# Optimization experiments

Hardware: AMD Instinct MI355X
Metric: run time of the kernel (lower is better)

## Reference

```python
import jax, jax.numpy as jnp
import numpy as np

N_TOKENS = 4096
HIDDEN = 2048
INTER = 1024
N_EXPERTS = 8          # routed experts
ZERO_EXPERTS = 2       # Longcat zero-computation (identity) experts
TOP_K = 2
ROUTED_SCALING = 2.5


def setup_inputs() -> dict:
    key = jax.random.key(0)
    k1, k2, k3, k4 = jax.random.split(key, 4)
    hidden_states = jax.random.normal(k1, (N_TOKENS, HIDDEN), dtype=jnp.float32)
    router_w = jax.random.normal(k2, (N_EXPERTS + ZERO_EXPERTS, HIDDEN), dtype=jnp.float32) * 0.02
    correction_bias = jnp.zeros((N_EXPERTS + ZERO_EXPERTS,), dtype=jnp.float32)
    # torch Linear weight layout [out, in]: gate_up [E, 2I, H], down [E, H, I]
    w_gate_up = jax.random.normal(k3, (N_EXPERTS, 2 * INTER, HIDDEN), dtype=jnp.float32) * 0.02
    w_down = jax.random.normal(k4, (N_EXPERTS, HIDDEN, INTER), dtype=jnp.float32) * 0.02
    return {
        'hidden_states': hidden_states,
        'router_w': router_w,
        'correction_bias': correction_bias,
        'w_gate_up': w_gate_up,
        'w_down': w_down,
    }


def reference(hidden_states, router_w, correction_bias, w_gate_up, w_down):
    x = hidden_states  # [N, H]
    # ---- router gemm (fp32, like dsv3_router_gemm) ----
    logits = jnp.einsum('nh,eh->ne', x.astype(jnp.float32), router_w)  # [N, E+Z]
    scores = jax.nn.sigmoid(logits)
    # biased top-k selection (sglang biased topk, renormalize=False)
    _, topk_idx = jax.lax.top_k(scores + correction_bias[None, :], TOP_K)  # [N, K]
    topk_w = jnp.take_along_axis(scores, topk_idx, axis=1)  # raw sigmoid scores
    # ---- combine weights per expert ----
    onehot = jax.nn.one_hot(topk_idx, N_EXPERTS + ZERO_EXPERTS, dtype=topk_w.dtype)  # [N,K,E+Z]
    combine = jnp.einsum('nke,nk->ne', onehot, topk_w)  # [N, E+Z]
    combine_real = combine[:, :N_EXPERTS]               # [N, E]
    w_zero = combine[:, N_EXPERTS:].sum(axis=-1)        # [N] identity-expert weight
    # ---- expert FFN (silu(gate) * up -> down), dense over experts ----
    gu = jnp.einsum('nh,efh->enf', x, w_gate_up)        # [E, N, 2I]
    gate, up = gu[..., :INTER], gu[..., INTER:]
    h = jax.nn.silu(gate) * up                          # [E, N, I]
    y = jnp.einsum('eni,ehi->enh', h, w_down)           # [E, N, H]
    out = jnp.einsum('enh,ne->nh', y, combine_real.astype(y.dtype))
    out = out + w_zero[:, None].astype(out.dtype) * x   # zero experts = identity
    return out * ROUTED_SCALING
```

## Files before the change

### kernel.cpp

```cpp
#include <hip/hip_runtime.h>
#include <cstdint>
#include <cstddef>

#define N_TOKENS 4096
#define HIDDEN   2048
#define INTER    1024
#define NE       8
#define NE_TOT   10
#define SCALE    2.5f

typedef short v8s __attribute__((ext_vector_type(8)));
typedef float v4f __attribute__((ext_vector_type(4)));

static __device__ inline int imin(int a, int b) { return a < b ? a : b; }

__device__ inline unsigned short f2bf(float f) {
  unsigned int u = __float_as_uint(f);
  u += 0x7fffu + ((u >> 16) & 1u);
  return (unsigned short)(u >> 16);
}

__device__ inline void gld_lds16(const void* g, void* l) {
  __builtin_amdgcn_global_load_lds(
      (const __attribute__((address_space(1))) unsigned int*)g,
      (__attribute__((address_space(3))) unsigned int*)l, 16, 0, 0);
}

__global__ __launch_bounds__(256) void cvt_all_kernel(
    const float* __restrict__ wgu, const float* __restrict__ wd,
    unsigned short* __restrict__ wgu_b, unsigned short* __restrict__ wd_b,
    int* __restrict__ counts) {
  if (blockIdx.x == 0 && threadIdx.x < NE) counts[threadIdx.x] = 0;
  int i = blockIdx.x * 256 + threadIdx.x;
  const int n8_gu = NE * 2 * INTER * HIDDEN / 8;
  const int n8_d  = NE * HIDDEN * INTER / 8;
  const float* src;
  unsigned short* dst;
  size_t b;
  if (i < n8_gu)            { src = wgu; dst = wgu_b; b = (size_t)i * 8; }
  else if (i < n8_gu + n8_d){ src = wd;  dst = wd_b;  b = (size_t)(i - n8_gu) * 8; }
  else return;
  float4 a0 = *(const float4*)(src + b);
  float4 a1 = *(const float4*)(src + b + 4);
  union { unsigned short u[8]; uint4 v; } r;
  r.u[0] = f2bf(a0.x); r.u[1] = f2bf(a0.y); r.u[2] = f2bf(a0.z); r.u[3] = f2bf(a0.w);
  r.u[4] = f2bf(a1.x); r.u[5] = f2bf(a1.y); r.u[6] = f2bf(a1.z); r.u[7] = f2bf(a1.w);
  *(uint4*)(dst + b) = r.v;
}

__global__ __launch_bounds__(256, 4) void router_kernel(
    const float* __restrict__ x, const float* __restrict__ rw,
    const float* __restrict__ bias, unsigned short* __restrict__ xb,
    int* __restrict__ counts, int* __restrict__ tok_list,
    int* __restrict__ tkp, float* __restrict__ tkw, float* __restrict__ out) {
  int tid  = threadIdx.x;
  int lane = tid & 63;
  int wid  = tid >> 6;
  int n    = blockIdx.x * 4 + wid;

  const float* xr = x + (size_t)n * HIDDEN;
  float acc[NE_TOT];
#pragma unroll
  for (int e = 0; e < NE_TOT; e++) acc[e] = 0.f;

#pragma unroll 1
  for (int i = 0; i < 8; i++) {
    int k = (i * 64 + lane) * 4;
    float4 xv = *(const float4*)(xr + k);
#pragma unroll
    for (int e = 0; e < NE_TOT; e++) {
      float4 w = *(const float4*)(rw + (size_t)e * HIDDEN + k);
      acc[e] += xv.x * w.x + xv.y * w.y + xv.z * w.z + xv.w * w.w;
    }
  }
#pragma unroll
  for (int e = 0; e < NE_TOT; e++) {
    float v = acc[e];
#pragma unroll
    for (int off = 32; off > 0; off >>= 1) v += __shfl_xor(v, off, 64);
    acc[e] = v;
  }

  float sc[NE_TOT], sb[NE_TOT];
#pragma unroll
  for (int e = 0; e < NE_TOT; e++) {
    sc[e] = 1.f / (1.f + expf(-acc[e]));
    sb[e] = sc[e] + bias[e];
  }
  int i1 = 0;
  for (int e = 1; e < NE_TOT; e++) if (sb[e] > sb[i1]) i1 = e;
  int i2 = (i1 == 0) ? 1 : 0;
  for (int e = 0; e < NE_TOT; e++) if (e != i1 && sb[e] > sb[i2]) i2 = e;
  float wzero = 0.f;
  if (i1 >= NE) wzero += sc[i1];
  if (i2 >= NE) wzero += sc[i2];
  if (lane == 0) {
#pragma unroll
    for (int tt = 0; tt < 2; tt++) {
      int idx = tt == 0 ? i1 : i2;
      int packed = 0;
      float w = 0.f;
      if (idx < NE) {
        int slot = atomicAdd(&counts[idx], 1);
        tok_list[idx * N_TOKENS + slot] = n;
        packed = (idx << 16) | slot;
        w = SCALE * sc[idx];
      }
      tkp[tt * N_TOKENS + n] = packed;
      tkw[tt * N_TOKENS + n] = w;
    }
  }
  float wz = SCALE * wzero;

#pragma unroll
  for (int i = 0; i < 8; i++) {
    int k = (i * 64 + lane) * 4;
    float4 xv = *(const float4*)(xr + k);
    ushort4 ob;
    ob.x = f2bf(xv.x); ob.y = f2bf(xv.y);
    ob.z = f2bf(xv.z); ob.w = f2bf(xv.w);
    *(ushort4*)(xb + (size_t)n * HIDDEN + k) = ob;
    float4 o;
    o.x = wz * xv.x; o.y = wz * xv.y; o.z = wz * xv.z; o.w = wz * xv.w;
    *(float4*)(out + (size_t)n * HIDDEN + k) = o;
  }
}

__global__ void offsets_kernel(const int* __restrict__ counts, int* __restrict__ offsets) {
  if (threadIdx.x == 0) {
    int s = 0;
    for (int e = 0; e < NE; e++) { offsets[e] = s; s += counts[e]; }
  }
}


__global__ __launch_bounds__(256, 2) void gateup_kernel(
    const unsigned short* __restrict__ xb, const unsigned short* __restrict__ wgu,
    const int* __restrict__ counts, const int* __restrict__ offsets,
    const int* __restrict__ tok_list, unsigned short* __restrict__ h_buf) {
  int jt = blockIdx.x;
  int mt = blockIdx.y;
  int e  = blockIdx.z;
  int count = counts[e];
  if (mt * 128 >= count) return;

  __shared__ unsigned short As[2][128 * 32];
  __shared__ unsigned short Bs[2][128 * 32];

  int tid  = threadIdx.x;
  int lane = tid & 63;
  int wm = (tid >> 7) & 1;
  int wn = (tid >> 6) & 1;

  int row0 = tid >> 2, row1 = row0 + 64;
  int col8 = (((tid & 3) ^ ((tid >> 3) & 3)) * 8);

  const int* tl = tok_list + e * N_TOKENS;
  int t0 = tl[imin(mt * 128 + row0, count - 1)];
  int t1 = tl[imin(mt * 128 + row1, count - 1)];
  const unsigned short* ag0 = xb + (size_t)t0 * HIDDEN + col8;
  const unsigned short* ag1 = xb + (size_t)t1 * HIDDEN + col8;

  int wn0 = row0 >> 6, wi0 = row0 & 63;
  int wn1 = row1 >> 6, wi1 = row1 & 63;
  int br0 = (wi0 < 32) ? (jt * 64 + wn0 * 32 + wi0) : (1024 + jt * 64 + wn0 * 32 + (wi0 - 32));
  int br1 = (wi1 < 32) ? (jt * 64 + wn1 * 32 + wi1) : (1024 + jt * 64 + wn1 * 32 + (wi1 - 32));
  const unsigned short* bbase = wgu + (size_t)e * (2 * INTER) * HIDDEN;
  const unsigned short* bg0 = bbase + (size_t)br0 * HIDDEN + col8;
  const unsigned short* bg1 = bbase + (size_t)br1 * HIDDEN + col8;

  v4f acc[4][4];
#pragma unroll
  for (int i = 0; i < 4; i++)
#pragma unroll
    for (int j = 0; j < 4; j++) acc[i][j] = v4f{0.f, 0.f, 0.f, 0.f};

  int mrow = wm * 64 + (lane & 15);
  int nrow = wn * 64 + (lane & 15);
  int kcol = (((lane >> 4) ^ ((lane >> 1) & 3)) * 8);

  gld_lds16(ag0, &As[0][(size_t)tid * 8]);
  gld_lds16(ag1, &As[0][2048 + (size_t)tid * 8]);
  gld_lds16(bg0, &Bs[0][(size_t)tid * 8]);
  gld_lds16(bg1, &Bs[0][2048 + (size_t)tid * 8]);
  ag0 += 32; ag1 += 32; bg0 += 32; bg1 += 32;
  __syncthreads();

  const int NK = HIDDEN / 32;
  for (int kt = 0; kt < NK; kt++) {
    int cur = kt & 1;
    if (kt + 1 < NK) {
      int nxt = cur ^ 1;
      gld_lds16(ag0, &As[nxt][(size_t)tid * 8]);
      gld_lds16(ag1, &As[nxt][2048 + (size_t)tid * 8]);
      gld_lds16(bg0, &Bs[nxt][(size_t)tid * 8]);
      gld_lds16(bg1, &Bs[nxt][2048 + (size_t)tid * 8]);
      ag0 += 32; ag1 += 32; bg0 += 32; bg1 += 32;
    }
    v8s a[4], b[4];
#pragma unroll
    for (int i = 0; i < 4; i++) a[i] = *(const v8s*)&As[cur][(mrow + i * 16) * 32 + kcol];
#pragma unroll
    for (int j = 0; j < 4; j++) b[j] = *(const v8s*)&Bs[cur][(nrow + j * 16) * 32 + kcol];
#pragma unroll
    for (int i = 0; i < 4; i++)
#pragma unroll
      for (int j = 0; j < 4; j++)
        acc[i][j] = __builtin_amdgcn_mfma_f32_16x16x32_bf16(a[i], b[j], acc[i][j], 0, 0, 0);
    __syncthreads();
  }

  int ocol  = lane & 15;
  int orow4 = (lane >> 4) * 4;
  int hoff  = offsets[e];
#pragma unroll
  for (int i = 0; i < 4; i++) {
#pragma unroll
    for (int r = 0; r < 4; r++) {
      int m = mt * 128 + wm * 64 + i * 16 + orow4 + r;
      if (m < count) {
        unsigned short* hrow = h_buf + (size_t)(hoff + m) * INTER;
#pragma unroll
        for (int j = 0; j < 2; j++) {
          float g = acc[i][j][r];
          float u = acc[i][j + 2][r];
          float hv = (g / (1.f + expf(-g))) * u;
          hrow[jt * 64 + wn * 32 + j * 16 + ocol] = f2bf(hv);
        }
      }
    }
  }
}

__global__ __launch_bounds__(256, 2) void down_kernel(
    const unsigned short* __restrict__ h_buf, const unsigned short* __restrict__ wd,
    const int* __restrict__ counts, const int* __restrict__ offsets,
    float* __restrict__ y_buf) {
  int nt = blockIdx.x;
  int mt = blockIdx.y;
  int e  = blockIdx.z;
  int count = counts[e];
  if (mt * 128 >= count) return;

  __shared__ unsigned short As[2][128 * 32];
  __shared__ unsigned short Bs[2][128 * 32];

  int tid  = threadIdx.x;
  int lane = tid & 63;
  int wm = (tid >> 7) & 1;
  int wn = (tid >> 6) & 1;

  int row0 = tid >> 2, row1 = row0 + 64;
  int col8 = (((tid & 3) ^ ((tid >> 3) & 3)) * 8);
  int hoff = offsets[e];

  const unsigned short* ag0 =
      h_buf + (size_t)(hoff + imin(mt * 128 + row0, count - 1)) * INTER + col8;
  const unsigned short* ag1 =
      h_buf + (size_t)(hoff + imin(mt * 128 + row1, count - 1)) * INTER + col8;
  const unsigned short* bbase = wd + (size_t)e * HIDDEN * INTER;
  const unsigned short* bg0 = bbase + (size_t)(nt * 128 + row0) * INTER + col8;
  const unsigned short* bg1 = bbase + (size_t)(nt * 128 + row1) * INTER + col8;

  v4f acc[4][4];
#pragma unroll
  for (int i = 0; i < 4; i++)
#pragma unroll
    for (int j = 0; j < 4; j++) acc[i][j] = v4f{0.f, 0.f, 0.f, 0.f};

  int mrow = wm * 64 + (lane & 15);
  int nrow = wn * 64 + (lane & 15);
  int kcol = (((lane >> 4) ^ ((lane >> 1) & 3)) * 8);

  gld_lds16(ag0, &As[0][(size_t)tid * 8]);
  gld_lds16(ag1, &As[0][2048 + (size_t)tid * 8]);
  gld_lds16(bg0, &Bs[0][(size_t)tid * 8]);
  gld_lds16(bg1, &Bs[0][2048 + (size_t)tid * 8]);
  ag0 += 32; ag1 += 32; bg0 += 32; bg1 += 32;
  __syncthreads();

  const int NK = INTER / 32;
  for (int kt = 0; kt < NK; kt++) {
    int cur = kt & 1;
    if (kt + 1 < NK) {
      int nxt = cur ^ 1;
      gld_lds16(ag0, &As[nxt][(size_t)tid * 8]);
      gld_lds16(ag1, &As[nxt][2048 + (size_t)tid * 8]);
      gld_lds16(bg0, &Bs[nxt][(size_t)tid * 8]);
      gld_lds16(bg1, &Bs[nxt][2048 + (size_t)tid * 8]);
      ag0 += 32; ag1 += 32; bg0 += 32; bg1 += 32;
    }
    v8s a[4], b[4];
#pragma unroll
    for (int i = 0; i < 4; i++) a[i] = *(const v8s*)&As[cur][(mrow + i * 16) * 32 + kcol];
#pragma unroll
    for (int j = 0; j < 4; j++) b[j] = *(const v8s*)&Bs[cur][(nrow + j * 16) * 32 + kcol];
#pragma unroll
    for (int i = 0; i < 4; i++)
#pragma unroll
      for (int j = 0; j < 4; j++)
        acc[i][j] = __builtin_amdgcn_mfma_f32_16x16x32_bf16(a[i], b[j], acc[i][j], 0, 0, 0);
    __syncthreads();
  }

  int ocol  = lane & 15;
  int orow4 = (lane >> 4) * 4;
#pragma unroll
  for (int i = 0; i < 4; i++) {
#pragma unroll
    for (int r = 0; r < 4; r++) {
      int m = mt * 128 + wm * 64 + i * 16 + orow4 + r;
      if (m < count) {
        float* yrow = y_buf + (size_t)(hoff + m) * HIDDEN + nt * 128 + wn * 64 + ocol;
#pragma unroll
        for (int j = 0; j < 4; j++) yrow[j * 16] = acc[i][j][r];
      }
    }
  }
}

__global__ __launch_bounds__(256, 4) void gather_kernel(
    const float* __restrict__ y_buf, const int* __restrict__ tkp,
    const float* __restrict__ tkw, const int* __restrict__ offsets,
    float* __restrict__ out) {
  int tid  = threadIdx.x;
  int lane = tid & 63;
  int wid  = tid >> 6;
  int n    = blockIdx.x * 4 + wid;

  int p1 = tkp[n], p2 = tkp[N_TOKENS + n];
  float w1 = tkw[n], w2 = tkw[N_TOKENS + n];
  const float* y1 = y_buf + (size_t)(offsets[p1 >> 16] + (p1 & 0xffff)) * HIDDEN;
  const float* y2 = y_buf + (size_t)(offsets[p2 >> 16] + (p2 & 0xffff)) * HIDDEN;
  float* orow = out + (size_t)n * HIDDEN;

#pragma unroll
  for (int i = 0; i < 8; i++) {
    int k = (i * 64 + lane) * 4;
    float4 o = *(const float4*)(orow + k);
    float4 a = *(const float4*)(y1 + k);
    float4 b = *(const float4*)(y2 + k);
    o.x += w1 * a.x + w2 * b.x;
    o.y += w1 * a.y + w2 * b.y;
    o.z += w1 * a.z + w2 * b.z;
    o.w += w1 * a.w + w2 * b.w;
    *(float4*)(orow + k) = o;
  }
}

extern "C" void kernel_launch(void* const* d_in, const int* in_sizes, int n_in,
                              void* d_out, int out_size, void* d_ws, size_t ws_size,
                              hipStream_t stream) {
  const float* x   = (const float*)d_in[0];
  const float* rw  = (const float*)d_in[1];
  const float* cb  = (const float*)d_in[2];
  const float* wgu = (const float*)d_in[3];
  const float* wd  = (const float*)d_in[4];
  float* out = (float*)d_out;

  char* ws = (char*)d_ws;
  size_t off = 0;
  auto alloc = [&](size_t bytes) {
    void* p = ws + off;
    off += (bytes + 255) & ~(size_t)255;
    return p;
  };
  unsigned short* xb    = (unsigned short*)alloc((size_t)N_TOKENS * HIDDEN * 2);
  unsigned short* wgu_b = (unsigned short*)alloc((size_t)NE * 2 * INTER * HIDDEN * 2);
  unsigned short* wd_b  = (unsigned short*)alloc((size_t)NE * HIDDEN * INTER * 2);
  unsigned short* h_buf = (unsigned short*)alloc((size_t)2 * N_TOKENS * INTER * 2);
  int*   tok_list = (int*)alloc((size_t)NE * N_TOKENS * 4);
  int*   tkp      = (int*)alloc((size_t)2 * N_TOKENS * 4);
  float* tkw      = (float*)alloc((size_t)2 * N_TOKENS * 4);
  int*   counts   = (int*)alloc(256);
  int*   offsets  = (int*)alloc(256);
  float* y_buf = (float*)wgu_b;
  (void)ws_size; (void)in_sizes; (void)n_in; (void)out_size;

  const int n8_total = (NE * 2 * INTER * HIDDEN + NE * HIDDEN * INTER) / 8;
  cvt_all_kernel<<<(n8_total + 255) / 256, 256, 0, stream>>>(wgu, wd, wgu_b, wd_b, counts);
  router_kernel<<<N_TOKENS / 4, 256, 0, stream>>>(x, rw, cb, xb, counts, tok_list, tkp, tkw, out);
  offsets_kernel<<<1, 64, 0, stream>>>(counts, offsets);
  gateup_kernel<<<dim3(16, 32, 8), 256, 0, stream>>>(xb, wgu_b, counts, offsets, tok_list, h_buf);
  down_kernel<<<dim3(16, 32, 8), 256, 0, stream>>>(h_buf, wd_b, counts, offsets, y_buf);
  gather_kernel<<<N_TOKENS / 4, 256, 0, stream>>>(y_buf, tkp, tkw, offsets, out);
}
```

Measured before the change: 516.7 us.

## Replace atomic token bucketing with deterministic single-block prefix-scan partition

The router no longer does global atomicAdd slot allocation. It writes each token's chosen expert ids as bytes. A new single-block partition kernel then counts tokens per expert with a shared-memory prefix scan and writes ordered token lists plus precomputed y_buf row indices, so the gather kernel drops its offsets lookup. This removes atomic contention and makes token order deterministic, which may improve locality in the expert GEMMs. The cost is a serialized one-block kernel with a 10-step scan over 32KB of shared memory.

After: 459.8 us. 11.0% less time.

```diff
diff --git a/kernel.cpp b/kernel.cpp
--- a/kernel.cpp
+++ b/kernel.cpp
@@ -28,9 +28,7 @@
 
 __global__ __launch_bounds__(256) void cvt_all_kernel(
     const float* __restrict__ wgu, const float* __restrict__ wd,
-    unsigned short* __restrict__ wgu_b, unsigned short* __restrict__ wd_b,
-    int* __restrict__ counts) {
-  if (blockIdx.x == 0 && threadIdx.x < NE) counts[threadIdx.x] = 0;
+    unsigned short* __restrict__ wgu_b, unsigned short* __restrict__ wd_b) {
   int i = blockIdx.x * 256 + threadIdx.x;
   const int n8_gu = NE * 2 * INTER * HIDDEN / 8;
   const int n8_d  = NE * HIDDEN * INTER / 8;
@@ -51,8 +49,8 @@
 __global__ __launch_bounds__(256, 4) void router_kernel(
     const float* __restrict__ x, const float* __restrict__ rw,
     const float* __restrict__ bias, unsigned short* __restrict__ xb,
-    int* __restrict__ counts, int* __restrict__ tok_list,
-    int* __restrict__ tkp, float* __restrict__ tkw, float* __restrict__ out) {
+    signed char* __restrict__ tke, float* __restrict__ tkw,
+    float* __restrict__ out) {
   int tid  = threadIdx.x;
   int lane = tid & 63;
   int wid  = tid >> 6;
@@ -95,20 +93,10 @@
   if (i1 >= NE) wzero += sc[i1];
   if (i2 >= NE) wzero += sc[i2];
   if (lane == 0) {
-#pragma unroll
-    for (int tt = 0; tt < 2; tt++) {
-      int idx = tt == 0 ? i1 : i2;
-      int packed = 0;
-      float w = 0.f;
-      if (idx < NE) {
-        int slot = atomicAdd(&counts[idx], 1);
-        tok_list[idx * N_TOKENS + slot] = n;
-        packed = (idx << 16) | slot;
-        w = SCALE * sc[idx];
-      }
-      tkp[tt * N_TOKENS + n] = packed;
-      tkw[tt * N_TOKENS + n] = w;
-    }
+    tke[n]            = (signed char)(i1 < NE ? i1 : -1);
+    tke[N_TOKENS + n] = (signed char)(i2 < NE ? i2 : -1);
+    tkw[n]            = i1 < NE ? SCALE * sc[i1] : 0.f;
+    tkw[N_TOKENS + n] = i2 < NE ? SCALE * sc[i2] : 0.f;
   }
   float wz = SCALE * wzero;
 
@@ -126,10 +114,74 @@
   }
 }
 
-__global__ void offsets_kernel(const int* __restrict__ counts, int* __restrict__ offsets) {
-  if (threadIdx.x == 0) {
+__global__ __launch_bounds__(1024) void partition_kernel(
+    const signed char* __restrict__ tke, int* __restrict__ tok_list,
+    int* __restrict__ tkr, int* __restrict__ counts, int* __restrict__ offsets) {
+  __shared__ int scn[1024][NE];
+  __shared__ int soff[NE];
+  int tid = threadIdx.x;
+  int t4  = tid * 4;
+
+  int w0 = *(const int*)(tke + t4);
+  int w1 = *(const int*)(tke + N_TOKENS + t4);
+
+#pragma unroll
+  for (int e = 0; e < NE; e++) scn[tid][e] = 0;
+#pragma unroll
+  for (int i = 0; i < 4; i++) {
+    int e0 = (int)(signed char)(w0 >> (8 * i));
+    int e1 = (int)(signed char)(w1 >> (8 * i));
+    if (e0 >= 0) scn[tid][e0]++;
+    if (e1 >= 0) scn[tid][e1]++;
+  }
+  int c[NE], orig[NE];
+#pragma unroll
+  for (int e = 0; e < NE; e++) { c[e] = scn[tid][e]; orig[e] = c[e]; }
+  __syncthreads();
+
+  for (int s = 1; s < 1024; s <<= 1) {
+    int v[NE];
+    bool act = (tid >= s);
+    if (act) {
+#pragma unroll
+      for (int e = 0; e < NE; e++) v[e] = scn[tid - s][e];
+    }
+    __syncthreads();
+    if (act) {
+#pragma unroll
+      for (int e = 0; e < NE; e++) { c[e] += v[e]; scn[tid][e] = c[e]; }
+    }
+    __syncthreads();
+  }
+
+  if (tid == 0) {
     int s = 0;
-    for (int e = 0; e < NE; e++) { offsets[e] = s; s += counts[e]; }
+#pragma unroll
+    for (int e = 0; e < NE; e++) {
+      int cnt = scn[1023][e];
+      counts[e] = cnt; offsets[e] = s; soff[e] = s; s += cnt;
+    }
+  }
+  __syncthreads();
+
+#pragma unroll
+  for (int e = 0; e < NE; e++) scn[tid][e] = c[e] - orig[e];
+
+#pragma unroll
+  for (int i = 0; i < 4; i++) {
+    int n  = t4 + i;
+    int e0 = (int)(signed char)(w0 >> (8 * i));
+    int e1 = (int)(signed char)(w1 >> (8 * i));
+    if (e0 >= 0) {
+      int slot = scn[tid][e0]++;
+      tok_list[e0 * N_TOKENS + slot] = n;
+      tkr[n] = soff[e0] + slot;
+    } else tkr[n] = 0;
+    if (e1 >= 0) {
+      int slot = scn[tid][e1]++;
+      tok_list[e1 * N_TOKENS + slot] = n;
+      tkr[N_TOKENS + n] = soff[e1] + slot;
+    } else tkr[N_TOKENS + n] = 0;
   }
 }
 
@@ -320,18 +372,17 @@
 }
 
 __global__ __launch_bounds__(256, 4) void gather_kernel(
-    const float* __restrict__ y_buf, const int* __restrict__ tkp,
-    const float* __restrict__ tkw, const int* __restrict__ offsets,
-    float* __restrict__ out) {
+    const float* __restrict__ y_buf, const int* __restrict__ tkr,
+    const float* __restrict__ tkw, float* __restrict__ out) {
   int tid  = threadIdx.x;
   int lane = tid & 63;
   int wid  = tid >> 6;
   int n    = blockIdx.x * 4 + wid;
 
-  int p1 = tkp[n], p2 = tkp[N_TOKENS + n];
+  int r1 = tkr[n], r2 = tkr[N_TOKENS + n];
   float w1 = tkw[n], w2 = tkw[N_TOKENS + n];
-  const float* y1 = y_buf + (size_t)(offsets[p1 >> 16] + (p1 & 0xffff)) * HIDDEN;
-  const float* y2 = y_buf + (size_t)(offsets[p2 >> 16] + (p2 & 0xffff)) * HIDDEN;
+  const float* y1 = y_buf + (size_t)r1 * HIDDEN;
+  const float* y2 = y_buf + (size_t)r2 * HIDDEN;
   float* orow = out + (size_t)n * HIDDEN;
 
 #pragma unroll
@@ -370,7 +421,8 @@
   unsigned short* wd_b  = (unsigned short*)alloc((size_t)NE * HIDDEN * INTER * 2);
   unsigned short* h_buf = (unsigned short*)alloc((size_t)2 * N_TOKENS * INTER * 2);
   int*   tok_list = (int*)alloc((size_t)NE * N_TOKENS * 4);
-  int*   tkp      = (int*)alloc((size_t)2 * N_TOKENS * 4);
+  signed char* tke = (signed char*)alloc((size_t)2 * N_TOKENS);
+  int*   tkr      = (int*)alloc((size_t)2 * N_TOKENS * 4);
   float* tkw      = (float*)alloc((size_t)2 * N_TOKENS * 4);
   int*   counts   = (int*)alloc(256);
   int*   offsets  = (int*)alloc(256);
@@ -378,10 +430,10 @@
   (void)ws_size; (void)in_sizes; (void)n_in; (void)out_size;
 
   const int n8_total = (NE * 2 * INTER * HIDDEN + NE * HIDDEN * INTER) / 8;
-  cvt_all_kernel<<<(n8_total + 255) / 256, 256, 0, stream>>>(wgu, wd, wgu_b, wd_b, counts);
-  router_kernel<<<N_TOKENS / 4, 256, 0, stream>>>(x, rw, cb, xb, counts, tok_list, tkp, tkw, out);
-  offsets_kernel<<<1, 64, 0, stream>>>(counts, offsets);
+  cvt_all_kernel<<<(n8_total + 255) / 256, 256, 0, stream>>>(wgu, wd, wgu_b, wd_b);
+  router_kernel<<<N_TOKENS / 4, 256, 0, stream>>>(x, rw, cb, xb, tke, tkw, out);
+  partition_kernel<<<1, 1024, 0, stream>>>(tke, tok_list, tkr, counts, offsets);
   gateup_kernel<<<dim3(16, 32, 8), 256, 0, stream>>>(xb, wgu_b, counts, offsets, tok_list, h_buf);
   down_kernel<<<dim3(16, 32, 8), 256, 0, stream>>>(h_buf, wd_b, counts, offsets, y_buf);
-  gather_kernel<<<N_TOKENS / 4, 256, 0, stream>>>(y_buf, tkp, tkw, offsets, out);
-}
+  gather_kernel<<<N_TOKENS / 4, 256, 0, stream>>>(y_buf, tkr, tkw, out);
+}
```
